# Kernel tuning notes

Hardware: AMD Instinct MI355X
Metric: run time of the kernel (lower is better)

Reference implementation:

```python
import jax, jax.numpy as jnp
import numpy as np

LENGTH = 512
Q = 2 * LENGTH + 3   # match + insert + flank/unannotated/terminal states
S = 26               # amino-acid alphabet size


def setup_inputs() -> dict:
    key = jax.random.key(0)
    k1, k2, k3, k4 = jax.random.split(key, 4)
    seq = jax.random.randint(k1, (256, 512), 0, S, dtype=jnp.int32)
    A_logits = jax.random.normal(k2, (Q, Q), dtype=jnp.float32)
    B_logits = jax.random.normal(k3, (Q, S), dtype=jnp.float32)
    init_logits = jax.random.normal(k4, (Q,), dtype=jnp.float32)
    return {"seq": seq, "A_logits": A_logits, "B_logits": B_logits,
            "init_logits": init_logits}


def reference(seq, A_logits, B_logits, init_logits):
    # Row-stochastic transition matrix A [q,q], emission matrix B [q,s],
    # initial state distribution init [q] (cell builds these from kernels
    # via softmax/normalization in make_A()/make_B()).
    A = jax.nn.softmax(A_logits, axis=-1)
    B = jax.nn.softmax(B_logits, axis=-1)
    init = jax.nn.softmax(init_logits)

    # Emission likelihoods per timestep: E[b,t,q] = B[q, seq[b,t]]
    E = B.T[seq]  # [batch, T, q]

    # Scaled HMM forward recursion (log-sum-exp in scaled prob space).
    alpha0 = init[None, :] * E[:, 0]            # [batch, q]
    s0 = jnp.sum(alpha0, axis=-1)               # [batch]
    carry0 = (alpha0 / s0[:, None], jnp.log(s0))

    def step(carry, e_t):
        alpha, ll = carry
        f = (alpha @ A) * e_t                   # [batch, q]
        s = jnp.sum(f, axis=-1)                 # scaling factor
        return (f / s[:, None], ll + jnp.log(s)), None

    E_rest = jnp.transpose(E[:, 1:], (1, 0, 2))  # [T-1, batch, q]
    (alpha, loglik), _ = jax.lax.scan(step, carry0, E_rest)
    return loglik  # per-sequence log-likelihood [batch]
```

## Files before the change

kernel.cpp:

```cpp
#include <hip/hip_runtime.h>
#include <math.h>

typedef __bf16 bf16x8 __attribute__((ext_vector_type(8)));
typedef float f32x4 __attribute__((ext_vector_type(4)));
typedef unsigned int u32x4 __attribute__((ext_vector_type(4)));
typedef unsigned long long u64;

constexpr int QQ = 1027;
constexpr int SS = 26;
constexpr int TT = 512;
constexpr int NB = 256;
constexpr int KP = 1056;
constexpr int NP = 1040;
constexpr int BTS = 1040;
constexpr int NSL = 13;
constexpr int NBB = 16;
constexpr int MB = 16;
constexpr int NWV = 5;
constexpr int CBLK = NWV * 64;
constexpr int KSTEPS = KP / 32;
constexpr int BUFN = NB * KP;
constexpr int RQ = KP / 4;
constexpr int LQ = RQ + 2;
constexpr int TOTQ = MB * RQ;
constexpr int NLD = TOTQ / CBLK;
constexpr int NREM = TOTQ - NLD * CBLK;
constexpr int PSE = NBB * NSL * MB;

__device__ __forceinline__ unsigned short f2bf(float f) {
  union { float f; unsigned u; } v; v.f = f;
  return (unsigned short)((v.u + 0x7fffu + ((v.u >> 16) & 1u)) >> 16);
}

__device__ __forceinline__ u64 ald8(const u64* p) {
  return __hip_atomic_load((u64*)p, __ATOMIC_RELAXED, __HIP_MEMORY_SCOPE_AGENT);
}
__device__ __forceinline__ void ast8(u64* p, u64 v) {
  __hip_atomic_store(p, v, __ATOMIC_RELAXED, __HIP_MEMORY_SCOPE_AGENT);
}

__device__ __forceinline__ float spin_tag(const u64* p, unsigned texp) {
  u64 v = ald8(p);
  while ((unsigned)(v >> 32) != texp) {
    __builtin_amdgcn_s_sleep(1);
    v = ald8(p);
  }
  union { unsigned u; float f; } w; w.u = (unsigned)v;
  return w.f;
}

__global__ void k_zero(u32x4* p, int n) {
  int i = blockIdx.x * blockDim.x + threadIdx.x;
  if (i < n) p[i] = (u32x4){0u, 0u, 0u, 0u};
}

__global__ void k_prep_init(const float* __restrict__ il, float* __restrict__ ip) {
  __shared__ float red[1024];
  int tid = threadIdx.x;
  float m = -1e30f;
  for (int q = tid; q < QQ; q += 1024) m = fmaxf(m, il[q]);
  red[tid] = m; __syncthreads();
  for (int off = 512; off > 0; off >>= 1) {
    if (tid < off) red[tid] = fmaxf(red[tid], red[tid + off]);
    __syncthreads();
  }
  m = red[0]; __syncthreads();
  float s = 0.f;
  for (int q = tid; q < QQ; q += 1024) s += expf(il[q] - m);
  red[tid] = s; __syncthreads();
  for (int off = 512; off > 0; off >>= 1) {
    if (tid < off) red[tid] += red[tid + off];
    __syncthreads();
  }
  s = red[0];
  float inv = 1.0f / s;
  for (int q = tid; q < QQ; q += 1024) ip[q] = expf(il[q] - m) * inv;
}

__global__ void k_prep_B(const float* __restrict__ bl, float* __restrict__ bt) {
  int q = blockIdx.x * blockDim.x + threadIdx.x;
  if (q >= QQ) return;
  const float* row = bl + (size_t)q * SS;
  float m = -1e30f;
  for (int c = 0; c < SS; ++c) m = fmaxf(m, row[c]);
  float s = 0.f;
  for (int c = 0; c < SS; ++c) s += expf(row[c] - m);
  float inv = 1.0f / s;
  for (int c = 0; c < SS; ++c) bt[c * BTS + q] = expf(row[c] - m) * inv;
}

__global__ void k_prep_A(const float* __restrict__ al, unsigned short* __restrict__ at) {
  int r = blockIdx.x;
  const float* row = al + (size_t)r * QQ;
  __shared__ float red[256];
  int tid = threadIdx.x;
  float m = -1e30f;
  for (int n = tid; n < QQ; n += 256) m = fmaxf(m, row[n]);
  red[tid] = m; __syncthreads();
  for (int off = 128; off > 0; off >>= 1) {
    if (tid < off) red[tid] = fmaxf(red[tid], red[tid + off]);
    __syncthreads();
  }
  m = red[0]; __syncthreads();
  float s = 0.f;
  for (int n = tid; n < QQ; n += 256) s += expf(row[n] - m);
  red[tid] = s; __syncthreads();
  for (int off = 128; off > 0; off >>= 1) {
    if (tid < off) red[tid] += red[tid + off];
    __syncthreads();
  }
  s = red[0];
  float inv = 1.0f / s;
  for (int n = tid; n < QQ; n += 256) at[(size_t)n * KP + r] = f2bf(expf(row[n] - m) * inv);
}

__global__ void k_init_step(const int* __restrict__ seq, const float* __restrict__ ip,
                            const float* __restrict__ Bt, unsigned short* __restrict__ buf0,
                            u64* __restrict__ psumE) {
  int b = blockIdx.x, tid = threadIdx.x;
  __shared__ float sp[16];
  if (tid < 16) sp[tid] = 0.f;
  __syncthreads();
  int c0 = seq[b * TT];
  for (int q = tid; q < NP; q += 256) {
    float v = ip[q] * Bt[c0 * BTS + q];
    buf0[(size_t)b * KP + q] = f2bf(v);
    atomicAdd(&sp[q / 80], v);
  }
  __syncthreads();
  if (tid < NSL) {
    union { float f; unsigned u; } w; w.f = sp[tid];
    psumE[(size_t)(b / MB) * (NSL * MB) + tid * MB + (b % MB)] = (u64)w.u;
  }
}

__global__ __launch_bounds__(CBLK, 1) void k_hmm_coop(
    const int* __restrict__ seq, const unsigned short* __restrict__ At,
    const float* __restrict__ Bt, unsigned short* __restrict__ bufB,
    u64* __restrict__ psumE, float* __restrict__ out) {
  __shared__ u64 aldsq[MB * LQ];
  __shared__ float srow[MB][NSL + 1];
  __shared__ float inv_lds[MB];
  __shared__ float spart[MB][NWV];

  const int tid = threadIdx.x, wg = blockIdx.x;
  const int bb = wg % NBB, sl = wg / NBB;
  const int lane = tid & 63, wv = tid >> 6;
  const int lrow = lane >> 4, lcol = lane & 15;
  const int n0w = (sl * NWV + wv) * 16;
  const int ssl = tid >> 4, srw = tid & 15;

  u32x4 atr[KSTEPS];
  {
    const u32x4* atp = (const u32x4*)(At + (size_t)(n0w + lcol) * KP + 8 * lrow);
#pragma unroll
    for (int ks = 0; ks < KSTEPS; ++ks) atr[ks] = atp[4 * ks];
#pragma unroll
    for (int ks = 0; ks < KSTEPS; ++ks) asm volatile("" : "+v"(atr[ks]));
  }

  float ll = 0.f;

  for (int t = 1; t < TT; ++t) {
    const int rd = (t - 1) % 3, wri = t % 3;
    const unsigned texp = (unsigned)(t - 1);
    const u64* tagb = psumE + ((size_t)rd * NBB + bb) * (NSL * MB);
    u64* tagw = psumE + ((size_t)wri * NBB + bb) * (NSL * MB);
    const u64* ain = (const u64*)(bufB + (size_t)rd * BUFN) + (size_t)bb * TOTQ;
    u64* wbuf8 = (u64*)(bufB + (size_t)wri * BUFN);

    const int ch = seq[(bb * MB + lcol) * TT + t];
    const f32x4 ev = *(const f32x4*)(Bt + (size_t)ch * BTS + n0w + 4 * lrow);

    if (tid < NSL * MB) srow[srw][ssl] = spin_tag(tagb + ssl * MB + srw, texp);
    __syncthreads();

    u64 av[NLD], avx = 0;
    const u64* asrc = ain + tid;
#pragma unroll
    for (int j = 0; j < NLD; ++j) av[j] = ald8(asrc + j * CBLK);
    if (tid < NREM) avx = ald8(asrc + NLD * CBLK);

#pragma unroll
    for (int j = 0; j < NLD; ++j) {
      int g = tid + j * CBLK;
      int r = g / RQ;
      aldsq[r * LQ + (g - r * RQ)] = av[j];
    }
    if (tid < NREM) {
      int g = tid + NLD * CBLK;
      int r = g / RQ;
      aldsq[r * LQ + (g - r * RQ)] = avx;
    }
    __syncthreads();

    const u32x4* ap = ((const u32x4*)aldsq) + lcol * (LQ / 2) + lrow;
    f32x4 acc = (f32x4){0.f, 0.f, 0.f, 0.f};
#pragma unroll
    for (int ks = 0; ks < KSTEPS; ++ks) {
      u32x4 af = ap[4 * ks];
      acc = __builtin_amdgcn_mfma_f32_16x16x32_bf16(
          __builtin_bit_cast(bf16x8, atr[ks]), __builtin_bit_cast(bf16x8, af),
          acc, 0, 0, 0);
    }

    if (tid < MB) {
      float s = 0.f;
#pragma unroll
      for (int c = 0; c < NSL; ++c) s += srow[tid][c];
      ll += logf(s);
      inv_lds[tid] = 1.0f / s;
    }
    __syncthreads();

    const float inv = inv_lds[lcol];
    float rs = 0.f;
    u64 hv = 0;
#pragma unroll
    for (int i = 0; i < 4; ++i) {
      float v = acc[i] * ev[i] * inv;
      rs += v;
      hv |= (u64)f2bf(v) << (16 * i);
    }
    ast8(wbuf8 + (size_t)(bb * MB + lcol) * RQ + (n0w >> 2) + lrow, hv);
    rs += __shfl_xor(rs, 16);
    rs += __shfl_xor(rs, 32);
    if (lane < 16) spart[lane][wv] = rs;
    asm volatile("s_waitcnt vmcnt(0)" ::: "memory");
    __syncthreads();

    if (tid < MB) {
      float s5 = spart[tid][0] + spart[tid][1] + spart[tid][2] +
                 spart[tid][3] + spart[tid][4];
      union { float f; unsigned u; } w; w.f = s5;
      ast8(tagw + sl * MB + tid, (u64)w.u | ((u64)(unsigned)t << 32));
    }
  }

  if (sl == 0) {
    const u64* tb = psumE + ((size_t)((TT - 1) % 3) * NBB + bb) * (NSL * MB);
    if (tid < NSL * MB)
      srow[srw][ssl] = spin_tag(tb + ssl * MB + srw, (unsigned)(TT - 1));
    __syncthreads();
    if (tid < MB) {
      float s = 0.f;
#pragma unroll
      for (int c = 0; c < NSL; ++c) s += srow[tid][c];
      out[bb * MB + tid] = ll + logf(s);
    }
  }
}

extern "C" void kernel_launch(void* const* d_in, const int* in_sizes, int n_in,
                              void* d_out, int out_size, void* d_ws, size_t ws_size,
                              hipStream_t stream) {
  const int* seq = (const int*)d_in[0];
  const float* Al = (const float*)d_in[1];
  const float* Bl = (const float*)d_in[2];
  const float* il = (const float*)d_in[3];
  float* out = (float*)d_out;

  char* ws = (char*)d_ws;
  unsigned short* At = (unsigned short*)ws;
  size_t off_bt = (size_t)NP * KP * 2;
  float* Bt = (float*)(ws + off_bt);
  size_t off_ip = off_bt + (size_t)SS * BTS * 4;
  float* ip = (float*)(ws + off_ip);
  size_t off_buf = off_ip + (size_t)NP * 4;
  unsigned short* bufB = (unsigned short*)(ws + off_buf);
  size_t off_ps = off_buf + (size_t)3 * BUFN * 2;
  u64* psumE = (u64*)(ws + off_ps);
  size_t total = off_ps + (size_t)3 * PSE * 8;
  int n16 = (int)((total + 15) / 16);

  k_zero<<<(n16 + 255) / 256, 256, 0, stream>>>((u32x4*)ws, n16);
  k_prep_init<<<1, 1024, 0, stream>>>(il, ip);
  k_prep_B<<<(QQ + 255) / 256, 256, 0, stream>>>(Bl, Bt);
  k_prep_A<<<QQ, 256, 0, stream>>>(Al, At);
  k_init_step<<<NB, 256, 0, stream>>>(seq, ip, Bt, bufB, psumE);

  void* args[] = {(void*)&seq, (void*)&At, (void*)&Bt, (void*)&bufB,
                  (void*)&psumE, (void*)&out};
  hipLaunchCooperativeKernel((void*)k_hmm_coop, dim3(NBB * NSL), dim3(CBLK),
                             args, 0, stream);
}
```

Before: 1.548 ms.

## Split K dimension across wave pairs and reduce partial MFMA accumulators via LDS

Doubles the waves per workgroup from 5 to 10 and splits each 16-column output tile's K reduction in half, with each wave of a pair holding half of the A columns in registers. The second wave writes its partial accumulator to shared memory, and the first wave adds it before scaling and storing. K padding grows to 1088 so it divides evenly into two halves of 17 MFMA steps. The aim is to shorten the serial MFMA chain on the per-timestep critical path and to spread the LDS-to-MFMA work over more waves. The cost is an extra barrier and an LDS round trip each step, plus slightly more padded K work.

```diff
diff --git a/kernel.cpp b/kernel.cpp
--- a/kernel.cpp
+++ b/kernel.cpp
@@ -10,15 +10,15 @@
 constexpr int SS = 26;
 constexpr int TT = 512;
 constexpr int NB = 256;
-constexpr int KP = 1056;
+constexpr int KP = 1088;
 constexpr int NP = 1040;
 constexpr int BTS = 1040;
 constexpr int NSL = 13;
 constexpr int NBB = 16;
 constexpr int MB = 16;
-constexpr int NWV = 5;
+constexpr int NWV = 10;
 constexpr int CBLK = NWV * 64;
-constexpr int KSTEPS = KP / 32;
+constexpr int KH = 17;
 constexpr int BUFN = NB * KP;
 constexpr int RQ = KP / 4;
 constexpr int LQ = RQ + 2;
@@ -139,24 +139,27 @@
     const float* __restrict__ Bt, unsigned short* __restrict__ bufB,
     u64* __restrict__ psumE, float* __restrict__ out) {
   __shared__ u64 aldsq[MB * LQ];
+  __shared__ f32x4 accred[5][64];
   __shared__ float srow[MB][NSL + 1];
   __shared__ float inv_lds[MB];
-  __shared__ float spart[MB][NWV];
+  __shared__ float spart[MB][5];
 
   const int tid = threadIdx.x, wg = blockIdx.x;
   const int bb = wg % NBB, sl = wg / NBB;
   const int lane = tid & 63, wv = tid >> 6;
+  const int p = wv >> 1, h = wv & 1;
   const int lrow = lane >> 4, lcol = lane & 15;
-  const int n0w = (sl * NWV + wv) * 16;
+  const int n0w = (sl * 5 + p) * 16;
   const int ssl = tid >> 4, srw = tid & 15;
 
-  u32x4 atr[KSTEPS];
+  u32x4 atr[KH];
   {
-    const u32x4* atp = (const u32x4*)(At + (size_t)(n0w + lcol) * KP + 8 * lrow);
-#pragma unroll
-    for (int ks = 0; ks < KSTEPS; ++ks) atr[ks] = atp[4 * ks];
-#pragma unroll
-    for (int ks = 0; ks < KSTEPS; ++ks) asm volatile("" : "+v"(atr[ks]));
+    const u32x4* atp =
+        (const u32x4*)(At + (size_t)(n0w + lcol) * KP + 8 * lrow) + (size_t)h * KH * 4;
+#pragma unroll
+    for (int j = 0; j < KH; ++j) atr[j] = atp[4 * j];
+#pragma unroll
+    for (int j = 0; j < KH; ++j) asm volatile("" : "+v"(atr[j]));
   }
 
   float ll = 0.f;
@@ -169,8 +172,11 @@
     const u64* ain = (const u64*)(bufB + (size_t)rd * BUFN) + (size_t)bb * TOTQ;
     u64* wbuf8 = (u64*)(bufB + (size_t)wri * BUFN);
 
-    const int ch = seq[(bb * MB + lcol) * TT + t];
-    const f32x4 ev = *(const f32x4*)(Bt + (size_t)ch * BTS + n0w + 4 * lrow);
+    f32x4 ev;
+    if (h == 0) {
+      const int ch = seq[(bb * MB + lcol) * TT + t];
+      ev = *(const f32x4*)(Bt + (size_t)ch * BTS + n0w + 4 * lrow);
+    }
 
     if (tid < NSL * MB) srow[srw][ssl] = spin_tag(tagb + ssl * MB + srw, texp);
     __syncthreads();
@@ -192,18 +198,6 @@
       int r = g / RQ;
       aldsq[r * LQ + (g - r * RQ)] = avx;
     }
-    __syncthreads();
-
-    const u32x4* ap = ((const u32x4*)aldsq) + lcol * (LQ / 2) + lrow;
-    f32x4 acc = (f32x4){0.f, 0.f, 0.f, 0.f};
-#pragma unroll
-    for (int ks = 0; ks < KSTEPS; ++ks) {
-      u32x4 af = ap[4 * ks];
-      acc = __builtin_amdgcn_mfma_f32_16x16x32_bf16(
-          __builtin_bit_cast(bf16x8, atr[ks]), __builtin_bit_cast(bf16x8, af),
-          acc, 0, 0, 0);
-    }
-
     if (tid < MB) {
       float s = 0.f;
 #pragma unroll
@@ -213,19 +207,36 @@
     }
     __syncthreads();
 
-    const float inv = inv_lds[lcol];
-    float rs = 0.f;
-    u64 hv = 0;
-#pragma unroll
-    for (int i = 0; i < 4; ++i) {
-      float v = acc[i] * ev[i] * inv;
-      rs += v;
-      hv |= (u64)f2bf(v) << (16 * i);
-    }
-    ast8(wbuf8 + (size_t)(bb * MB + lcol) * RQ + (n0w >> 2) + lrow, hv);
-    rs += __shfl_xor(rs, 16);
-    rs += __shfl_xor(rs, 32);
-    if (lane < 16) spart[lane][wv] = rs;
+    const u32x4* ap =
+        ((const u32x4*)aldsq) + lcol * (LQ / 2) + lrow + (size_t)h * KH * 4;
+    f32x4 acc = (f32x4){0.f, 0.f, 0.f, 0.f};
+#pragma unroll
+    for (int j = 0; j < KH; ++j) {
+      u32x4 af = ap[4 * j];
+      acc = __builtin_amdgcn_mfma_f32_16x16x32_bf16(
+          __builtin_bit_cast(bf16x8, atr[j]), __builtin_bit_cast(bf16x8, af),
+          acc, 0, 0, 0);
+    }
+
+    if (h == 1) accred[p][lane] = acc;
+    __syncthreads();
+
+    if (h == 0) {
+      const f32x4 other = accred[p][lane];
+      const float inv = inv_lds[lcol];
+      float rs = 0.f;
+      u64 hv = 0;
+#pragma unroll
+      for (int i = 0; i < 4; ++i) {
+        float v = (acc[i] + other[i]) * ev[i] * inv;
+        rs += v;
+        hv |= (u64)f2bf(v) << (16 * i);
+      }
+      ast8(wbuf8 + (size_t)(bb * MB + lcol) * RQ + (n0w >> 2) + lrow, hv);
+      rs += __shfl_xor(rs, 16);
+      rs += __shfl_xor(rs, 32);
+      if (lane < 16) spart[lane][p] = rs;
+    }
     asm volatile("s_waitcnt vmcnt(0)" ::: "memory");
     __syncthreads();
 
```

After: 1.672 ms. 8.0% more time.

## Compute row sums via ones-MFMA and replace partial-sum exchange with per-wave tags

Applied to the files above, without the earlier changes.

Each step's normaliser is now taken from an extra MFMA that multiplies a ones matrix by the previous alpha tile already in LDS. This removes the cross-workgroup partial-sum exchange, two of the per-step __syncthreads, and the shuffle reductions. Each wave now publishes its own ready tag, and the final log-likelihood sums the last alpha buffer directly. In exchange the MFMA count per step doubles, and the normaliser is computed from bf16-rounded alpha rather than fp32 partial sums, which changes precision slightly.

```diff
diff --git a/kernel.cpp b/kernel.cpp
--- a/kernel.cpp
+++ b/kernel.cpp
@@ -21,11 +21,12 @@
 constexpr int KSTEPS = KP / 32;
 constexpr int BUFN = NB * KP;
 constexpr int RQ = KP / 4;
-constexpr int LQ = RQ + 2;
+constexpr int LQ = 274;
 constexpr int TOTQ = MB * RQ;
 constexpr int NLD = TOTQ / CBLK;
 constexpr int NREM = TOTQ - NLD * CBLK;
-constexpr int PSE = NBB * NSL * MB;
+constexpr int NTAG = NSL * NWV;
+constexpr int TSTR = 80;
 
 __device__ __forceinline__ unsigned short f2bf(float f) {
   union { float f; unsigned u; } v; v.f = f;
@@ -39,14 +40,22 @@
   __hip_atomic_store(p, v, __ATOMIC_RELAXED, __HIP_MEMORY_SCOPE_AGENT);
 }
 
-__device__ __forceinline__ float spin_tag(const u64* p, unsigned texp) {
+__device__ __forceinline__ void spin_tag(const u64* p, unsigned texp) {
   u64 v = ald8(p);
   while ((unsigned)(v >> 32) != texp) {
     __builtin_amdgcn_s_sleep(1);
     v = ald8(p);
   }
-  union { unsigned u; float f; } w; w.u = (unsigned)v;
-  return w.f;
+}
+
+__device__ __forceinline__ float sum4bf(u64 q) {
+  union { unsigned u; float f; } a, b, c, d;
+  a.u = ((unsigned)(q & 0xFFFFu)) << 16;
+  b.u = (unsigned)(q >> 16) << 16;
+  b.u = ((unsigned)((q >> 16) & 0xFFFFu)) << 16;
+  c.u = ((unsigned)((q >> 32) & 0xFFFFu)) << 16;
+  d.u = ((unsigned)((q >> 48) & 0xFFFFu)) << 16;
+  return (a.f + b.f) + (c.f + d.f);
 }
 
 __global__ void k_zero(u32x4* p, int n) {
@@ -115,64 +124,48 @@
 }
 
 __global__ void k_init_step(const int* __restrict__ seq, const float* __restrict__ ip,
-                            const float* __restrict__ Bt, unsigned short* __restrict__ buf0,
-                            u64* __restrict__ psumE) {
+                            const float* __restrict__ Bt, unsigned short* __restrict__ buf0) {
   int b = blockIdx.x, tid = threadIdx.x;
-  __shared__ float sp[16];
-  if (tid < 16) sp[tid] = 0.f;
-  __syncthreads();
   int c0 = seq[b * TT];
-  for (int q = tid; q < NP; q += 256) {
-    float v = ip[q] * Bt[c0 * BTS + q];
-    buf0[(size_t)b * KP + q] = f2bf(v);
-    atomicAdd(&sp[q / 80], v);
-  }
-  __syncthreads();
-  if (tid < NSL) {
-    union { float f; unsigned u; } w; w.f = sp[tid];
-    psumE[(size_t)(b / MB) * (NSL * MB) + tid * MB + (b % MB)] = (u64)w.u;
-  }
+  for (int q = tid; q < NP; q += 256)
+    buf0[(size_t)b * KP + q] = f2bf(ip[q] * Bt[c0 * BTS + q]);
 }
 
 __global__ __launch_bounds__(CBLK, 1) void k_hmm_coop(
     const int* __restrict__ seq, const unsigned short* __restrict__ At,
     const float* __restrict__ Bt, unsigned short* __restrict__ bufB,
-    u64* __restrict__ psumE, float* __restrict__ out) {
+    u64* __restrict__ tagsE, float* __restrict__ out) {
   __shared__ u64 aldsq[MB * LQ];
-  __shared__ float srow[MB][NSL + 1];
-  __shared__ float inv_lds[MB];
-  __shared__ float spart[MB][NWV];
+  __shared__ float srowF[MB];
 
   const int tid = threadIdx.x, wg = blockIdx.x;
   const int bb = wg % NBB, sl = wg / NBB;
   const int lane = tid & 63, wv = tid >> 6;
   const int lrow = lane >> 4, lcol = lane & 15;
   const int n0w = (sl * NWV + wv) * 16;
-  const int ssl = tid >> 4, srw = tid & 15;
 
   u32x4 atr[KSTEPS];
   {
     const u32x4* atp = (const u32x4*)(At + (size_t)(n0w + lcol) * KP + 8 * lrow);
 #pragma unroll
     for (int ks = 0; ks < KSTEPS; ++ks) atr[ks] = atp[4 * ks];
-#pragma unroll
-    for (int ks = 0; ks < KSTEPS; ++ks) asm volatile("" : "+v"(atr[ks]));
-  }
+  }
+  const u32x4 ones4 = (u32x4){0x3F803F80u, 0x3F803F80u, 0x3F803F80u, 0x3F803F80u};
 
   float ll = 0.f;
 
   for (int t = 1; t < TT; ++t) {
     const int rd = (t - 1) % 3, wri = t % 3;
     const unsigned texp = (unsigned)(t - 1);
-    const u64* tagb = psumE + ((size_t)rd * NBB + bb) * (NSL * MB);
-    u64* tagw = psumE + ((size_t)wri * NBB + bb) * (NSL * MB);
+    const u64* tagb = tagsE + ((size_t)rd * NBB + bb) * TSTR;
+    u64* tagw = tagsE + ((size_t)wri * NBB + bb) * TSTR;
     const u64* ain = (const u64*)(bufB + (size_t)rd * BUFN) + (size_t)bb * TOTQ;
     u64* wbuf8 = (u64*)(bufB + (size_t)wri * BUFN);
 
     const int ch = seq[(bb * MB + lcol) * TT + t];
     const f32x4 ev = *(const f32x4*)(Bt + (size_t)ch * BTS + n0w + 4 * lrow);
 
-    if (tid < NSL * MB) srow[srw][ssl] = spin_tag(tagb + ssl * MB + srw, texp);
+    if (tid < NTAG) spin_tag(tagb + tid, texp);
     __syncthreads();
 
     u64 av[NLD], avx = 0;
@@ -196,58 +189,51 @@
 
     const u32x4* ap = ((const u32x4*)aldsq) + lcol * (LQ / 2) + lrow;
     f32x4 acc = (f32x4){0.f, 0.f, 0.f, 0.f};
+    f32x4 accs = (f32x4){0.f, 0.f, 0.f, 0.f};
 #pragma unroll
     for (int ks = 0; ks < KSTEPS; ++ks) {
       u32x4 af = ap[4 * ks];
       acc = __builtin_amdgcn_mfma_f32_16x16x32_bf16(
           __builtin_bit_cast(bf16x8, atr[ks]), __builtin_bit_cast(bf16x8, af),
           acc, 0, 0, 0);
-    }
-
-    if (tid < MB) {
-      float s = 0.f;
-#pragma unroll
-      for (int c = 0; c < NSL; ++c) s += srow[tid][c];
-      ll += logf(s);
-      inv_lds[tid] = 1.0f / s;
-    }
-    __syncthreads();
-
-    const float inv = inv_lds[lcol];
-    float rs = 0.f;
+      accs = __builtin_amdgcn_mfma_f32_16x16x32_bf16(
+          __builtin_bit_cast(bf16x8, ones4), __builtin_bit_cast(bf16x8, af),
+          accs, 0, 0, 0);
+    }
+
+    const float s = accs[0];
+    const float inv = 1.0f / s;
+    if (sl == 0 && wv == 0) ll += logf(s);
+
     u64 hv = 0;
 #pragma unroll
     for (int i = 0; i < 4; ++i) {
       float v = acc[i] * ev[i] * inv;
-      rs += v;
       hv |= (u64)f2bf(v) << (16 * i);
     }
     ast8(wbuf8 + (size_t)(bb * MB + lcol) * RQ + (n0w >> 2) + lrow, hv);
-    rs += __shfl_xor(rs, 16);
-    rs += __shfl_xor(rs, 32);
-    if (lane < 16) spart[lane][wv] = rs;
     asm volatile("s_waitcnt vmcnt(0)" ::: "memory");
-    __syncthreads();
-
-    if (tid < MB) {
-      float s5 = spart[tid][0] + spart[tid][1] + spart[tid][2] +
-                 spart[tid][3] + spart[tid][4];
-      union { float f; unsigned u; } w; w.f = s5;
-      ast8(tagw + sl * MB + tid, (u64)w.u | ((u64)(unsigned)t << 32));
-    }
+    if (lane == 0) ast8(tagw + sl * NWV + wv, (u64)(unsigned)t << 32);
   }
 
   if (sl == 0) {
-    const u64* tb = psumE + ((size_t)((TT - 1) % 3) * NBB + bb) * (NSL * MB);
-    if (tid < NSL * MB)
-      srow[srw][ssl] = spin_tag(tb + ssl * MB + srw, (unsigned)(TT - 1));
-    __syncthreads();
-    if (tid < MB) {
-      float s = 0.f;
-#pragma unroll
-      for (int c = 0; c < NSL; ++c) s += srow[tid][c];
-      out[bb * MB + tid] = ll + logf(s);
-    }
+    if (tid < MB) srowF[tid] = 0.f;
+    const int fs = (TT - 1) % 3;
+    const u64* tagb = tagsE + ((size_t)fs * NBB + bb) * TSTR;
+    if (tid < NTAG) spin_tag(tagb + tid, (unsigned)(TT - 1));
+    __syncthreads();
+    const u64* ain = (const u64*)(bufB + (size_t)fs * BUFN) + (size_t)bb * TOTQ;
+#pragma unroll
+    for (int j = 0; j < NLD; ++j) {
+      int g = tid + j * CBLK;
+      atomicAdd(&srowF[g / RQ], sum4bf(ald8(ain + g)));
+    }
+    if (tid < NREM) {
+      int g = tid + NLD * CBLK;
+      atomicAdd(&srowF[g / RQ], sum4bf(ald8(ain + g)));
+    }
+    __syncthreads();
+    if (wv == 0 && lrow == 0) out[bb * MB + lcol] = ll + logf(srowF[lcol]);
   }
 }
 
@@ -268,19 +254,19 @@
   float* ip = (float*)(ws + off_ip);
   size_t off_buf = off_ip + (size_t)NP * 4;
   unsigned short* bufB = (unsigned short*)(ws + off_buf);
-  size_t off_ps = off_buf + (size_t)3 * BUFN * 2;
-  u64* psumE = (u64*)(ws + off_ps);
-  size_t total = off_ps + (size_t)3 * PSE * 8;
+  size_t off_tag = off_buf + (size_t)3 * BUFN * 2;
+  u64* tagsE = (u64*)(ws + off_tag);
+  size_t total = off_tag + (size_t)3 * NBB * TSTR * 8;
   int n16 = (int)((total + 15) / 16);
 
   k_zero<<<(n16 + 255) / 256, 256, 0, stream>>>((u32x4*)ws, n16);
   k_prep_init<<<1, 1024, 0, stream>>>(il, ip);
   k_prep_B<<<(QQ + 255) / 256, 256, 0, stream>>>(Bl, Bt);
   k_prep_A<<<QQ, 256, 0, stream>>>(Al, At);
-  k_init_step<<<NB, 256, 0, stream>>>(seq, ip, Bt, bufB, psumE);
+  k_init_step<<<NB, 256, 0, stream>>>(seq, ip, Bt, bufB);
 
   void* args[] = {(void*)&seq, (void*)&At, (void*)&Bt, (void*)&bufB,
-                  (void*)&psumE, (void*)&out};
+                  (void*)&tagsE, (void*)&out};
   hipLaunchCooperativeKernel((void*)k_hmm_coop, dim3(NBB * NSL), dim3(CBLK),
                              args, 0, stream);
 }
```

Measured after the change: 1.625 ms. 1.05x slower.
